# Optimization experiments

Measured on AMD Instinct MI355X. Metric: run time of the kernel, lower is better.

Reference implementation:

```python
import jax, jax.numpy as jnp
import numpy as np

B, N, L = 128, 100, 30
D_FEAT, C, CMD, T = 2112, 512, 512, 4
NEG = -1e30
INV_SQRT_C = np.float32(1.0 / np.sqrt(C))


def setup_inputs() -> dict:
    key = jax.random.key(0)
    ks = iter(jax.random.split(key, 64))

    def lin(out, inn):
        s = 1.0 / np.sqrt(inn)
        W = jax.random.uniform(next(ks), (out, inn), minval=-s, maxval=s, dtype=jnp.float32)
        b = jax.random.uniform(next(ks), (out,), minval=-s, maxval=s, dtype=jnp.float32)
        return W, b

    inp = {}
    inp['images'] = jax.random.normal(next(ks), (B, N, D_FEAT), dtype=jnp.float32)
    inp['q_encoding'] = jax.random.normal(next(ks), (B, CMD), dtype=jnp.float32)
    inp['lstm_outputs'] = jax.random.normal(next(ks), (B, L, CMD), dtype=jnp.float32)
    inp['W_initKB'], inp['b_initKB'] = lin(C, D_FEAT)
    inp['initMem'] = jax.random.normal(next(ks), (1, 1, C), dtype=jnp.float32)
    inp['W_qIn'], inp['b_qIn'] = lin(CMD, CMD)
    Ws, bs = zip(*[lin(CMD, CMD) for _ in range(T)])
    inp['W_qIn2'] = jnp.stack(Ws)
    inp['b_qIn2'] = jnp.stack(bs)
    inp['W_logit'], inp['b_logit'] = lin(1, CMD)
    inp['W_ploc'], inp['b_ploc'] = lin(C, C)
    inp['W_pctx'], inp['b_pctx'] = lin(C, C)
    inp['W_q'], inp['b_q'] = lin(C, 3 * C)
    inp['W_k'], inp['b_k'] = lin(C, 3 * C)
    inp['W_v'], inp['b_v'] = lin(C, 3 * C)
    inp['W_pk'], inp['b_pk'] = lin(C, CMD)
    inp['W_pv'], inp['b_pv'] = lin(C, CMD)
    inp['W_mem'], inp['b_mem'] = lin(C, 2 * C)
    inp['W_comb'], inp['b_comb'] = lin(C, 2 * C)
    inp['q_length'] = jax.random.randint(next(ks), (B,), 1, L + 1)
    inp['entity_num'] = jax.random.randint(next(ks), (B,), 1, N + 1)
    return inp


def _linear(x, W, b):
    return x @ W.T + b


def reference(images, q_encoding, lstm_outputs, W_initKB, b_initKB, initMem,
              W_qIn, b_qIn, W_qIn2, b_qIn2, W_logit, b_logit,
              W_ploc, b_ploc, W_pctx, b_pctx, W_q, b_q, W_k, b_k, W_v, b_v,
              W_pk, b_pk, W_pv, b_pv, W_mem, b_mem, W_comb, b_comb,
              q_length, entity_num):
    # stem (STEM_LINEAR + STEM_NORMALIZE); eval mode so dropouts + var-drop mask are identity
    imgs = images / jnp.maximum(jnp.linalg.norm(images, axis=-1, keepdims=True), 1e-12)
    x_loc = _linear(imgs, W_initKB, b_initKB)                              # [B,N,C]
    x_ctx = jnp.broadcast_to(initMem, x_loc.shape)                         # [B,N,C]
    q_mask = jnp.arange(L)[None, :] < q_length[:, None]                    # apply_mask1d [B,L]
    k_mask = jnp.arange(N)[None, None, :] < entity_num[:, None, None]      # apply_mask2d [B,1,N]
    q_cmd_base = jax.nn.elu(_linear(q_encoding, W_qIn, b_qIn))             # shared qInput layer
    for t in range(T):
        # extract textual command
        q_cmd = _linear(q_cmd_base, W_qIn2[t], b_qIn2[t])                  # [B,CMD]
        raw_att = _linear(q_cmd[:, None, :] * lstm_outputs, W_logit, b_logit)[..., 0]  # [B,L]
        att = jax.nn.softmax(jnp.where(q_mask, raw_att, NEG), axis=-1)
        cmd = jnp.einsum('bl,blc->bc', att, lstm_outputs)                  # [B,CMD]
        # propagate message
        proj_loc = _linear(x_loc, W_ploc, b_ploc)
        proj_ctx = _linear(x_ctx, W_pctx, b_pctx)
        x_joint = jnp.concatenate([x_loc, x_ctx, proj_loc * proj_ctx], axis=-1)  # [B,N,3C]
        queries = _linear(x_joint, W_q, b_q)
        keys = _linear(x_joint, W_k, b_k) * _linear(cmd, W_pk, b_pk)[:, None, :]
        vals = _linear(x_joint, W_v, b_v) * _linear(cmd, W_pv, b_pv)[:, None, :]
        scores = jnp.einsum('bqc,bkc->bqk', queries, keys) * INV_SQRT_C    # [B,N,N]
        prob = jax.nn.softmax(jnp.where(k_mask, scores, NEG), axis=-1)
        message = jnp.einsum('bqk,bkc->bqc', prob, vals)
        x_ctx = _linear(jnp.concatenate([x_ctx, message], axis=-1), W_mem, b_mem)
    return _linear(jnp.concatenate([x_loc, x_ctx], axis=-1), W_comb, b_comb)
```

## Files before the change

### kernel.cpp

```cpp
#include <hip/hip_runtime.h>
#include <math.h>

#define BB 128
#define NN 100
#define LL 30
#define CC 512
#define DFEAT 2112
#define TT 4
#define ROWS (BB * NN)
#define XJLD 1536
#define INV_SQRT_C_F 0.04419417382415922f
#define QH 50
#define VTK 128

typedef __attribute__((ext_vector_type(8))) short short8;
typedef __attribute__((ext_vector_type(4))) float f32x4;

__device__ inline unsigned short f2bf(float f) {
    unsigned u = __float_as_uint(f);
    u += 0x7fff + ((u >> 16) & 1);
    return (unsigned short)(u >> 16);
}
__device__ inline float b2f(unsigned short h) { return __uint_as_float((unsigned)h << 16); }

__device__ inline void async_ld16(const unsigned short* g, unsigned short* l) {
    __builtin_amdgcn_global_load_lds((const __attribute__((address_space(1))) void*)g,
                                     (__attribute__((address_space(3))) void*)l, 16, 0, 0);
}

__global__ __launch_bounds__(256) void rownorm_kernel(const float* __restrict__ img,
                                                      float* __restrict__ inv_norm) {
    int r = blockIdx.x;
    const float* p = img + (size_t)r * DFEAT;
    float s = 0.f;
    for (int i = threadIdx.x; i < DFEAT; i += 256) { float v = p[i]; s += v * v; }
    __shared__ float red[4];
    int lane = threadIdx.x & 63, wid = threadIdx.x >> 6;
#pragma unroll
    for (int off = 32; off > 0; off >>= 1) s += __shfl_down(s, off);
    if (lane == 0) red[wid] = s;
    __syncthreads();
    if (threadIdx.x == 0) {
        float tot = red[0] + red[1] + red[2] + red[3];
        inv_norm[r] = 1.f / fmaxf(sqrtf(tot), 1e-12f);
    }
}

__global__ __launch_bounds__(256) void cvt_kernel(const float* __restrict__ s,
                                                  unsigned short* __restrict__ d, int n4) {
    int i = blockIdx.x * blockDim.x + threadIdx.x;
    if (i < n4) {
        float4 v = ((const float4*)s)[i];
        ushort4 o;
        o.x = f2bf(v.x); o.y = f2bf(v.y); o.z = f2bf(v.z); o.w = f2bf(v.w);
        ((ushort4*)d)[i] = o;
    }
}

__global__ void zero16_kernel(uint4* __restrict__ p, int n) {
    int i = blockIdx.x * blockDim.x + threadIdx.x;
    if (i < n) p[i] = uint4{0u, 0u, 0u, 0u};
}

__global__ void bcast_kernel(const float* __restrict__ m, unsigned short* __restrict__ x) {
    int i = blockIdx.x * blockDim.x + threadIdx.x;
    if (i < ROWS * CC) {
        int r = i >> 9, c = i & (CC - 1);
        x[(size_t)r * XJLD + CC + c] = f2bf(m[c]);
    }
}

template <int MODE, bool AF32, bool OUTF32, bool DUAL, bool VT>
__global__ __launch_bounds__(256) void gemm_mfma(
    const void* __restrict__ A_, int lda,
    const unsigned short* __restrict__ W, int ldw,
    const float* __restrict__ bias,
    void* __restrict__ C_, int ldc,
    void* __restrict__ C2_,
    int K,
    const float* __restrict__ arsc,
    const float* __restrict__ rowscale) {
    __shared__ unsigned short As[128 * 64];
    __shared__ unsigned short Bs[128 * 64];
    const int t = threadIdx.x;
    const int l = t & 63;
    const int wv = t >> 6;
    const int wr = wv >> 1, wc = wv & 1;
    const int lg = l >> 4, lm = l & 15;
    const int nwg = gridDim.x;
    const int qq = nwg >> 3, rr = nwg & 7;
    const int xcd = blockIdx.x & 7, idx = blockIdx.x >> 3;
    const int wgid = (xcd < rr ? xcd * (qq + 1) : rr * (qq + 1) + (xcd - rr) * qq) + idx;
    const int m0 = (wgid >> 2) * 128, n0 = (wgid & 3) * 128;

    f32x4 acc[4][4];
#pragma unroll
    for (int mi = 0; mi < 4; ++mi)
#pragma unroll
        for (int ni = 0; ni < 4; ++ni) acc[mi][ni] = {0.f, 0.f, 0.f, 0.f};

    for (int k0 = 0; k0 < K; k0 += 64) {
        if (AF32) {
            const float* Af = (const float*)A_;
            int row = t >> 1, half = t & 1;
            const float* s = Af + (size_t)(m0 + row) * lda + k0 + half * 32;
            float sc = arsc ? arsc[m0 + row] : 1.f;
#pragma unroll
            for (int c = 0; c < 4; ++c) {
                float4 v0 = *(const float4*)(s + c * 8);
                float4 v1 = *(const float4*)(s + c * 8 + 4);
                short8 h;
                h[0] = (short)f2bf(v0.x * sc); h[1] = (short)f2bf(v0.y * sc);
                h[2] = (short)f2bf(v0.z * sc); h[3] = (short)f2bf(v0.w * sc);
                h[4] = (short)f2bf(v1.x * sc); h[5] = (short)f2bf(v1.y * sc);
                h[6] = (short)f2bf(v1.z * sc); h[7] = (short)f2bf(v1.w * sc);
                int cs = half * 4 + c;
                *(short8*)&As[row * 64 + ((cs ^ (row & 7)) * 8)] = h;
            }
        } else {
            const unsigned short* Ah = (const unsigned short*)A_;
#pragma unroll
            for (int i = 0; i < 4; ++i) {
                int lin = t + i * 256;
                int row = lin >> 3, seg = lin & 7;
                async_ld16(Ah + (size_t)(m0 + row) * lda + k0 + ((seg ^ (row & 7)) * 8),
                           &As[lin * 8]);
            }
        }
#pragma unroll
        for (int i = 0; i < 4; ++i) {
            int lin = t + i * 256;
            int row = lin >> 3, seg = lin & 7;
            async_ld16(W + (size_t)(n0 + row) * ldw + k0 + ((seg ^ (row & 7)) * 8),
                       &Bs[lin * 8]);
        }
        __syncthreads();

#pragma unroll
        for (int kk = 0; kk < 2; ++kk) {
            short8 af[4], bq[4];
#pragma unroll
            for (int mi = 0; mi < 4; ++mi) {
                int row = wr * 64 + mi * 16 + lm;
                int cs = kk * 4 + lg;
                af[mi] = *(const short8*)&As[row * 64 + ((cs ^ (row & 7)) * 8)];
            }
#pragma unroll
            for (int ni = 0; ni < 4; ++ni) {
                int row = wc * 64 + ni * 16 + lm;
                int cs = kk * 4 + lg;
                bq[ni] = *(const short8*)&Bs[row * 64 + ((cs ^ (row & 7)) * 8)];
            }
#pragma unroll
            for (int mi = 0; mi < 4; ++mi)
#pragma unroll
                for (int ni = 0; ni < 4; ++ni)
                    acc[mi][ni] = __builtin_amdgcn_mfma_f32_16x16x32_bf16(af[mi], bq[ni], acc[mi][ni], 0, 0, 0);
        }
        __syncthreads();
    }

#pragma unroll
    for (int mi = 0; mi < 4; ++mi) {
        int rbase = m0 + wr * 64 + mi * 16 + lg * 4;
#pragma unroll
        for (int ni = 0; ni < 4; ++ni) {
            int n = n0 + wc * 64 + ni * 16 + lm;
            float bv = bias[n];
#pragma unroll
            for (int j = 0; j < 4; ++j) {
                int r = rbase + j;
                float v = acc[mi][ni][j] + bv;
                size_t off = (size_t)r * ldc + n;
                if (MODE == 2) v *= b2f(((const unsigned short*)C_)[off]);
                if (MODE == 3) v *= rowscale[(size_t)(r / NN) * CC + n];
                if (OUTF32) {
                    ((float*)C_)[off] = v;
                } else {
                    unsigned short hv = f2bf(v);
                    if (VT) {
                        int b2 = r / NN, rl = r - b2 * NN;
                        ((unsigned short*)C_)[((size_t)b2 * CC + n) * VTK + rl] = hv;
                    } else {
                        ((unsigned short*)C_)[off] = hv;
                        if (DUAL) ((unsigned short*)C2_)[off] = hv;
                    }
                }
            }
        }
    }
}

template <int MODE>
__global__ __launch_bounds__(256) void gemm_small(
    const float* __restrict__ A, const float* __restrict__ W,
    const float* __restrict__ bias, float* __restrict__ C) {
    __shared__ float As[32 * 72];
    __shared__ float Bs[32 * 72];
    const int t = threadIdx.x;
    const int m0 = blockIdx.x * 64, n0 = blockIdx.y * 64;
    const int tr = t >> 4, tc = t & 15;
    float acc[4][4];
#pragma unroll
    for (int i = 0; i < 4; ++i)
#pragma unroll
        for (int j = 0; j < 4; ++j) acc[i][j] = 0.f;

    for (int k0 = 0; k0 < CC; k0 += 32) {
        int row = t >> 2, seg = t & 3;
        {
            const float* s = A + (size_t)(m0 + row) * CC + k0 + seg * 8;
            float4 v0 = *(const float4*)s, v1 = *(const float4*)(s + 4);
            As[(seg * 8 + 0) * 72 + row] = v0.x; As[(seg * 8 + 1) * 72 + row] = v0.y;
            As[(seg * 8 + 2) * 72 + row] = v0.z; As[(seg * 8 + 3) * 72 + row] = v0.w;
            As[(seg * 8 + 4) * 72 + row] = v1.x; As[(seg * 8 + 5) * 72 + row] = v1.y;
            As[(seg * 8 + 6) * 72 + row] = v1.z; As[(seg * 8 + 7) * 72 + row] = v1.w;
        }
        {
            const float* s = W + (size_t)(n0 + row) * CC + k0 + seg * 8;
            float4 v0 = *(const float4*)s, v1 = *(const float4*)(s + 4);
            Bs[(seg * 8 + 0) * 72 + row] = v0.x; Bs[(seg * 8 + 1) * 72 + row] = v0.y;
            Bs[(seg * 8 + 2) * 72 + row] = v0.z; Bs[(seg * 8 + 3) * 72 + row] = v0.w;
            Bs[(seg * 8 + 4) * 72 + row] = v1.x; Bs[(seg * 8 + 5) * 72 + row] = v1.y;
            Bs[(seg * 8 + 6) * 72 + row] = v1.z; Bs[(seg * 8 + 7) * 72 + row] = v1.w;
        }
        __syncthreads();
#pragma unroll
        for (int kk = 0; kk < 32; ++kk) {
            float4 a = *(const float4*)&As[kk * 72 + tr * 4];
            float4 b = *(const float4*)&Bs[kk * 72 + tc * 4];
            float av[4] = {a.x, a.y, a.z, a.w}, bv[4] = {b.x, b.y, b.z, b.w};
#pragma unroll
            for (int i = 0; i < 4; ++i)
#pragma unroll
                for (int j = 0; j < 4; ++j) acc[i][j] = fmaf(av[i], bv[j], acc[i][j]);
        }
        __syncthreads();
    }
#pragma unroll
    for (int i = 0; i < 4; ++i) {
#pragma unroll
        for (int j = 0; j < 4; ++j) {
            int n = n0 + tc * 4 + j;
            float v = acc[i][j] + bias[n];
            if (MODE == 4) v = v > 0.f ? v : expm1f(v);
            C[(size_t)(m0 + tr * 4 + i) * CC + n] = v;
        }
    }
}

__global__ __launch_bounds__(256) void cmd_kernel(
    const float* __restrict__ qcmd, const float* __restrict__ lstm,
    const float* __restrict__ wlogit, const float* __restrict__ blogit,
    const int* __restrict__ qlen, float* __restrict__ cmd) {
    const int b = blockIdx.x;
    const int t = threadIdx.x;
    __shared__ float qw[CC];
    __shared__ float att[LL];
    for (int c = t; c < CC; c += 256) qw[c] = qcmd[b * CC + c] * wlogit[c];
    __syncthreads();
    const int wid = t >> 6, lane = t & 63;
    for (int l = wid; l < LL; l += 4) {
        const float* lp = lstm + ((size_t)b * LL + l) * CC;
        float s = 0.f;
        for (int c = lane; c < CC; c += 64) s = fmaf(qw[c], lp[c], s);
#pragma unroll
        for (int off = 32; off > 0; off >>= 1) s += __shfl_down(s, off);
        if (lane == 0) att[l] = s + blogit[0];
    }
    __syncthreads();
    if (t == 0) {
        int Lq = qlen[b];
        float mx = -1e30f;
        for (int l = 0; l < LL; ++l) {
            if (l >= Lq) att[l] = -1e30f;
            mx = fmaxf(mx, att[l]);
        }
        float sum = 0.f;
        for (int l = 0; l < LL; ++l) { float e = expf(att[l] - mx); att[l] = e; sum += e; }
        float inv = 1.f / sum;
        for (int l = 0; l < LL; ++l) att[l] *= inv;
    }
    __syncthreads();
    for (int c = t; c < CC; c += 256) {
        float s = 0.f;
        for (int l = 0; l < LL; ++l) s = fmaf(att[l], lstm[((size_t)b * LL + l) * CC + c], s);
        cmd[b * CC + c] = s;
    }
}

__global__ __launch_bounds__(256) void attn_mfma_kernel(
    const unsigned short* __restrict__ Qm, const unsigned short* __restrict__ Km,
    const unsigned short* __restrict__ Vt, const int* __restrict__ entnum,
    unsigned short* __restrict__ msg) {
    __shared__ char ldsraw[64 * 132 * 4];
    float* S = (float*)ldsraw;
    unsigned short* Qs = (unsigned short*)ldsraw;
    unsigned short* Ks = (unsigned short*)(ldsraw + 8192);
    const int b = blockIdx.x;
    const int qbase = blockIdx.y * QH;
    const int t = threadIdx.x;
    const int wv = t >> 6, l = t & 63, lg = l >> 4, lm = l & 15;
    const unsigned short* Qp = Qm + ((size_t)b * NN + qbase) * CC;
    const unsigned short* Kp = Km + (size_t)b * NN * CC;

    f32x4 sacc[7];
#pragma unroll
    for (int i = 0; i < 7; ++i) sacc[i] = {0.f, 0.f, 0.f, 0.f};

    for (int k0 = 0; k0 < CC; k0 += 64) {
#pragma unroll
        for (int i = 0; i < 2; ++i) {
            int lin = t + i * 256;
            int row = lin >> 3, seg = lin & 7;
            async_ld16(Qp + (size_t)row * CC + k0 + ((seg ^ (row & 7)) * 8), &Qs[lin * 8]);
        }
#pragma unroll
        for (int i = 0; i < 4; ++i) {
            int lin = t + i * 256;
            if (lin < 896) {
                int row = lin >> 3, seg = lin & 7;
                async_ld16(Kp + (size_t)row * CC + k0 + ((seg ^ (row & 7)) * 8), &Ks[lin * 8]);
            }
        }
        __syncthreads();
#pragma unroll
        for (int kk = 0; kk < 2; ++kk) {
            int arow = wv * 16 + lm;
            int cs = kk * 4 + lg;
            short8 a = *(const short8*)&Qs[arow * 64 + ((cs ^ (arow & 7)) * 8)];
#pragma unroll
            for (int nf = 0; nf < 7; ++nf) {
                int brow = nf * 16 + lm;
                short8 bb = *(const short8*)&Ks[brow * 64 + ((cs ^ (brow & 7)) * 8)];
                sacc[nf] = __builtin_amdgcn_mfma_f32_16x16x32_bf16(a, bb, sacc[nf], 0, 0, 0);
            }
        }
        __syncthreads();
    }
#pragma unroll
    for (int nf = 0; nf < 7; ++nf)
#pragma unroll
        for (int j = 0; j < 4; ++j)
            S[(wv * 16 + lg * 4 + j) * 132 + nf * 16 + lm] = sacc[nf][j] * INV_SQRT_C_F;
    __syncthreads();

    const int en = entnum[b];
    for (int q = wv; q < QH; q += 4) {
        float v0 = (l < en) ? S[q * 132 + l] : -1e30f;
        int k1 = l + 64;
        float v1 = (k1 < en) ? S[q * 132 + k1] : -1e30f;
        float mx = fmaxf(v0, v1);
#pragma unroll
        for (int o = 32; o > 0; o >>= 1) mx = fmaxf(mx, __shfl_xor(mx, o));
        float e0 = (l < en) ? expf(v0 - mx) : 0.f;
        float e1 = (k1 < en) ? expf(v1 - mx) : 0.f;
        float ss = e0 + e1;
#pragma unroll
        for (int o = 32; o > 0; o >>= 1) ss += __shfl_xor(ss, o);
        float inv = 1.f / ss;
        S[q * 132 + l] = e0 * inv;
        S[q * 132 + k1] = e1 * inv;
    }
    __syncthreads();

    f32x4 acc[4][8];
#pragma unroll
    for (int mf = 0; mf < 4; ++mf)
#pragma unroll
        for (int nf = 0; nf < 8; ++nf) acc[mf][nf] = {0.f, 0.f, 0.f, 0.f};

    const unsigned short* Vb = Vt + (size_t)b * CC * VTK;
    for (int ks = 0; ks < 4; ++ks) {
        int k0 = ks * 32;
        short8 pa[4];
#pragma unroll
        for (int mf = 0; mf < 4; ++mf) {
            const float* sp = &S[(mf * 16 + lm) * 132 + k0 + lg * 8];
            short8 h;
#pragma unroll
            for (int jj = 0; jj < 8; ++jj) h[jj] = (short)f2bf(sp[jj]);
            pa[mf] = h;
        }
#pragma unroll
        for (int nf = 0; nf < 8; ++nf) {
            short8 bb = *(const short8*)(Vb + ((size_t)(wv * 128 + nf * 16 + lm)) * VTK + k0 + lg * 8);
#pragma unroll
            for (int mf = 0; mf < 4; ++mf)
                acc[mf][nf] = __builtin_amdgcn_mfma_f32_16x16x32_bf16(pa[mf], bb, acc[mf][nf], 0, 0, 0);
        }
    }
#pragma unroll
    for (int mf = 0; mf < 4; ++mf) {
#pragma unroll
        for (int j = 0; j < 4; ++j) {
            int q = mf * 16 + lg * 4 + j;
            if (q < QH) {
                size_t rb = ((size_t)b * NN + qbase + q) * XJLD;
#pragma unroll
                for (int nf = 0; nf < 8; ++nf)
                    msg[rb + wv * 128 + nf * 16 + lm] = f2bf(acc[mf][nf][j]);
            }
        }
    }
}

extern "C" void kernel_launch(void* const* d_in, const int* in_sizes, int n_in,
                              void* d_out, int out_size, void* d_ws, size_t ws_size,
                              hipStream_t stream) {
    const float* images   = (const float*)d_in[0];
    const float* q_enc    = (const float*)d_in[1];
    const float* lstm     = (const float*)d_in[2];
    const float* W_initKB = (const float*)d_in[3];
    const float* b_initKB = (const float*)d_in[4];
    const float* initMem  = (const float*)d_in[5];
    const float* W_qIn    = (const float*)d_in[6];
    const float* b_qIn    = (const float*)d_in[7];
    const float* W_qIn2   = (const float*)d_in[8];
    const float* b_qIn2   = (const float*)d_in[9];
    const float* W_logit  = (const float*)d_in[10];
    const float* b_logit  = (const float*)d_in[11];
    const float* W_ploc   = (const float*)d_in[12];
    const float* b_ploc   = (const float*)d_in[13];
    const float* W_pctx   = (const float*)d_in[14];
    const float* b_pctx   = (const float*)d_in[15];
    const float* W_q      = (const float*)d_in[16];
    const float* b_q      = (const float*)d_in[17];
    const float* W_k      = (const float*)d_in[18];
    const float* b_k      = (const float*)d_in[19];
    const float* W_v      = (const float*)d_in[20];
    const float* b_v      = (const float*)d_in[21];
    const float* W_pk     = (const float*)d_in[22];
    const float* b_pk     = (const float*)d_in[23];
    const float* W_pv     = (const float*)d_in[24];
    const float* b_pv     = (const float*)d_in[25];
    const float* W_mem    = (const float*)d_in[26];
    const float* b_mem    = (const float*)d_in[27];
    const float* W_comb   = (const float*)d_in[28];
    const float* b_comb   = (const float*)d_in[29];
    const int* q_length   = (const int*)d_in[30];
    const int* entity_num = (const int*)d_in[31];
    (void)in_sizes; (void)n_in; (void)out_size; (void)ws_size;

    char* p = (char*)d_ws;
    auto alloc = [&](size_t bytes) { char* q = p; p += (bytes + 255) & ~(size_t)255; return q; };
    unsigned short* XJ0 = (unsigned short*)alloc((size_t)ROWS * XJLD * 2);
    unsigned short* XJ1 = (unsigned short*)alloc((size_t)ROWS * XJLD * 2);
    unsigned short* Qb  = (unsigned short*)alloc((size_t)ROWS * CC * 2);
    unsigned short* Kb  = (unsigned short*)alloc((size_t)ROWS * CC * 2);
    unsigned short* Vt  = (unsigned short*)alloc((size_t)BB * CC * VTK * 2);
    unsigned short* Wbf = (unsigned short*)alloc((size_t)5013504 * 2);
    float* qcb  = (float*)alloc((size_t)BB * CC * 4);
    float* qcmd = (float*)alloc((size_t)BB * CC * 4);
    float* cmd  = (float*)alloc((size_t)BB * CC * 4);
    float* pk   = (float*)alloc((size_t)BB * CC * 4);
    float* pv   = (float*)alloc((size_t)BB * CC * 4);
    float* invn = (float*)alloc((size_t)ROWS * 4);

    unsigned short* Wi_init = Wbf + 0;
    unsigned short* Wi_ploc = Wbf + 1081344;
    unsigned short* Wi_pctx = Wbf + 1343488;
    unsigned short* Wi_q    = Wbf + 1605632;
    unsigned short* Wi_k    = Wbf + 2392064;
    unsigned short* Wi_v    = Wbf + 3178496;
    unsigned short* Wi_mem  = Wbf + 3964928;
    unsigned short* Wi_comb = Wbf + 4489216;

    auto cvt = [&](const float* src, unsigned short* dst, size_t n) {
        int n4 = (int)(n / 4);
        cvt_kernel<<<dim3((n4 + 255) / 256), dim3(256), 0, stream>>>(src, dst, n4);
    };

    rownorm_kernel<<<dim3(ROWS), dim3(256), 0, stream>>>(images, invn);
    zero16_kernel<<<dim3(((int)((size_t)BB * CC * VTK * 2 / 16) + 255) / 256), dim3(256), 0, stream>>>(
        (uint4*)Vt, (int)((size_t)BB * CC * VTK * 2 / 16));
    cvt(W_initKB, Wi_init, (size_t)CC * DFEAT);
    cvt(W_ploc,  Wi_ploc, (size_t)CC * CC);
    cvt(W_pctx,  Wi_pctx, (size_t)CC * CC);
    cvt(W_q,     Wi_q,    (size_t)CC * 3 * CC);
    cvt(W_k,     Wi_k,    (size_t)CC * 3 * CC);
    cvt(W_v,     Wi_v,    (size_t)CC * 3 * CC);
    cvt(W_mem,   Wi_mem,  (size_t)CC * 2 * CC);
    cvt(W_comb,  Wi_comb, (size_t)CC * 2 * CC);

    dim3 gBig((ROWS / 128) * 4), blk(256);
    gemm_mfma<0, true, false, true, false><<<gBig, blk, 0, stream>>>(
        images, DFEAT, Wi_init, DFEAT, b_initKB, XJ0, XJLD, XJ1, DFEAT, invn, nullptr);
    bcast_kernel<<<dim3((ROWS * CC + 255) / 256), dim3(256), 0, stream>>>(initMem, XJ0);
    gemm_small<4><<<dim3(BB / 64, 8), blk, 0, stream>>>(q_enc, W_qIn, b_qIn, qcb);

    for (int t = 0; t < TT; ++t) {
        unsigned short* R  = (t & 1) ? XJ1 : XJ0;
        unsigned short* Wr = (t & 1) ? XJ0 : XJ1;
        gemm_small<0><<<dim3(BB / 64, 8), blk, 0, stream>>>(
            qcb, W_qIn2 + (size_t)t * CC * CC, b_qIn2 + (size_t)t * CC, qcmd);
        cmd_kernel<<<dim3(BB), blk, 0, stream>>>(qcmd, lstm, W_logit, b_logit, q_length, cmd);
        gemm_small<0><<<dim3(BB / 64, 8), blk, 0, stream>>>(cmd, W_pk, b_pk, pk);
        gemm_small<0><<<dim3(BB / 64, 8), blk, 0, stream>>>(cmd, W_pv, b_pv, pv);
        gemm_mfma<0, false, false, false, false><<<gBig, blk, 0, stream>>>(
            R, XJLD, Wi_ploc, CC, b_ploc, R + 2 * CC, XJLD, nullptr, CC, nullptr, nullptr);
        gemm_mfma<2, false, false, false, false><<<gBig, blk, 0, stream>>>(
            R + CC, XJLD, Wi_pctx, CC, b_pctx, R + 2 * CC, XJLD, nullptr, CC, nullptr, nullptr);
        gemm_mfma<0, false, false, false, false><<<gBig, blk, 0, stream>>>(
            R, XJLD, Wi_q, 3 * CC, b_q, Qb, CC, nullptr, 3 * CC, nullptr, nullptr);
        gemm_mfma<3, false, false, false, false><<<gBig, blk, 0, stream>>>(
            R, XJLD, Wi_k, 3 * CC, b_k, Kb, CC, nullptr, 3 * CC, nullptr, pk);
        gemm_mfma<3, false, false, false, true><<<gBig, blk, 0, stream>>>(
            R, XJLD, Wi_v, 3 * CC, b_v, Vt, CC, nullptr, 3 * CC, nullptr, pv);
        attn_mfma_kernel<<<dim3(BB, 2), blk, 0, stream>>>(Qb, Kb, Vt, entity_num, R + 2 * CC);
        gemm_mfma<0, false, false, false, false><<<gBig, blk, 0, stream>>>(
            R + CC, XJLD, Wi_mem, 2 * CC, b_mem, Wr + CC, XJLD, nullptr, 2 * CC, nullptr, nullptr);
    }
    gemm_mfma<0, false, true, false, false><<<gBig, blk, 0, stream>>>(
        XJ0, XJLD, Wi_comb, 2 * CC, b_comb, (float*)d_out, CC, nullptr, 2 * CC, nullptr, nullptr);
}
```

Baseline: 1.575 ms.

## Fuse ploc/pctx product GEMM, merge Q/K/V GEMMs, add double-buffered LDS

The ploc and pctx projections now run in one kernel that keeps two accumulators and writes their product directly, so the separate read-modify-write pass is gone. The Q, K and V projections become a single launch with a 12-way tile split, which removes launch gaps and gives a larger grid. The bf16 GEMMs now double-buffer LDS staging so the next K tile loads while the current one computes. The cost is twice the LDS per block and, in the product kernel, twice the accumulator registers, which may lower occupancy.

Result: no change. 1.569 ms (-0.4%).

```diff
diff --git a/kernel.cpp b/kernel.cpp
--- a/kernel.cpp
+++ b/kernel.cpp
@@ -28,6 +28,12 @@
                                      (__attribute__((address_space(3))) void*)l, 16, 0, 0);
 }
 
+__device__ inline int xcd_swz(int bid, int nwg) {
+    int qq = nwg >> 3, rr = nwg & 7;
+    int xcd = bid & 7, idx = bid >> 3;
+    return (xcd < rr ? xcd * (qq + 1) : rr * (qq + 1) + (xcd - rr) * qq) + idx;
+}
+
 __global__ __launch_bounds__(256) void rownorm_kernel(const float* __restrict__ img,
                                                       float* __restrict__ inv_norm) {
     int r = blockIdx.x;
@@ -70,16 +76,275 @@
     }
 }
 
-template <int MODE, bool AF32, bool OUTF32, bool DUAL, bool VT>
-__global__ __launch_bounds__(256) void gemm_mfma(
-    const void* __restrict__ A_, int lda,
+template <int EPI>
+__global__ __launch_bounds__(256) void gemm_dbuf(
+    const unsigned short* __restrict__ A, int lda,
     const unsigned short* __restrict__ W, int ldw,
     const float* __restrict__ bias,
-    void* __restrict__ C_, int ldc,
-    void* __restrict__ C2_,
-    int K,
-    const float* __restrict__ arsc,
-    const float* __restrict__ rowscale) {
+    void* __restrict__ C_, int ldc, int K) {
+    __shared__ unsigned short As[2][128 * 64];
+    __shared__ unsigned short Bs[2][128 * 64];
+    const int t = threadIdx.x;
+    const int l = t & 63;
+    const int wv = t >> 6;
+    const int wr = wv >> 1, wc = wv & 1;
+    const int lg = l >> 4, lm = l & 15;
+    const int wgid = xcd_swz(blockIdx.x, gridDim.x);
+    const int m0 = (wgid >> 2) * 128, n0 = (wgid & 3) * 128;
+
+    f32x4 acc[4][4];
+#pragma unroll
+    for (int mi = 0; mi < 4; ++mi)
+#pragma unroll
+        for (int ni = 0; ni < 4; ++ni) acc[mi][ni] = {0.f, 0.f, 0.f, 0.f};
+
+    auto stage = [&](int buf, int k0) {
+#pragma unroll
+        for (int i = 0; i < 4; ++i) {
+            int lin = t + i * 256;
+            int row = lin >> 3, seg = lin & 7;
+            async_ld16(A + (size_t)(m0 + row) * lda + k0 + ((seg ^ (row & 7)) * 8),
+                       &As[buf][lin * 8]);
+            async_ld16(W + (size_t)(n0 + row) * ldw + k0 + ((seg ^ (row & 7)) * 8),
+                       &Bs[buf][lin * 8]);
+        }
+    };
+
+    const int nk = K >> 6;
+    stage(0, 0);
+    __syncthreads();
+    for (int kt = 0; kt < nk; ++kt) {
+        int cur = kt & 1;
+        if (kt + 1 < nk) stage(cur ^ 1, (kt + 1) * 64);
+#pragma unroll
+        for (int kk = 0; kk < 2; ++kk) {
+            short8 af[4], bq[4];
+#pragma unroll
+            for (int mi = 0; mi < 4; ++mi) {
+                int row = wr * 64 + mi * 16 + lm;
+                int cs = kk * 4 + lg;
+                af[mi] = *(const short8*)&As[cur][row * 64 + ((cs ^ (row & 7)) * 8)];
+            }
+#pragma unroll
+            for (int ni = 0; ni < 4; ++ni) {
+                int row = wc * 64 + ni * 16 + lm;
+                int cs = kk * 4 + lg;
+                bq[ni] = *(const short8*)&Bs[cur][row * 64 + ((cs ^ (row & 7)) * 8)];
+            }
+#pragma unroll
+            for (int mi = 0; mi < 4; ++mi)
+#pragma unroll
+                for (int ni = 0; ni < 4; ++ni)
+                    acc[mi][ni] = __builtin_amdgcn_mfma_f32_16x16x32_bf16(af[mi], bq[ni], acc[mi][ni], 0, 0, 0);
+        }
+        __syncthreads();
+    }
+
+#pragma unroll
+    for (int mi = 0; mi < 4; ++mi) {
+        int rbase = m0 + wr * 64 + mi * 16 + lg * 4;
+#pragma unroll
+        for (int ni = 0; ni < 4; ++ni) {
+            int n = n0 + wc * 64 + ni * 16 + lm;
+            float bv = bias[n];
+#pragma unroll
+            for (int j = 0; j < 4; ++j) {
+                int r = rbase + j;
+                float v = acc[mi][ni][j] + bv;
+                if (EPI == 1) ((float*)C_)[(size_t)r * ldc + n] = v;
+                else ((unsigned short*)C_)[(size_t)r * ldc + n] = f2bf(v);
+            }
+        }
+    }
+}
+
+__global__ __launch_bounds__(256) void gemm_qkv(
+    const unsigned short* __restrict__ A,
+    const unsigned short* __restrict__ Wq, const unsigned short* __restrict__ Wk,
+    const unsigned short* __restrict__ Wv,
+    const float* __restrict__ bq_, const float* __restrict__ bk_,
+    const float* __restrict__ bv_,
+    unsigned short* __restrict__ Qb, unsigned short* __restrict__ Kb,
+    unsigned short* __restrict__ Vt,
+    const float* __restrict__ pk, const float* __restrict__ pv) {
+    __shared__ unsigned short As[2][128 * 64];
+    __shared__ unsigned short Bs[2][128 * 64];
+    const int t = threadIdx.x;
+    const int l = t & 63;
+    const int wv_ = t >> 6;
+    const int wr = wv_ >> 1, wc = wv_ & 1;
+    const int lg = l >> 4, lm = l & 15;
+    const int wgid = xcd_swz(blockIdx.x, gridDim.x);
+    const int mtile = wgid / 12, sub = wgid - mtile * 12;
+    const int op = sub >> 2;
+    const int m0 = mtile * 128, n0 = (sub & 3) * 128;
+    const unsigned short* W = (op == 0) ? Wq : (op == 1) ? Wk : Wv;
+    const float* bias = (op == 0) ? bq_ : (op == 1) ? bk_ : bv_;
+
+    f32x4 acc[4][4];
+#pragma unroll
+    for (int mi = 0; mi < 4; ++mi)
+#pragma unroll
+        for (int ni = 0; ni < 4; ++ni) acc[mi][ni] = {0.f, 0.f, 0.f, 0.f};
+
+    auto stage = [&](int buf, int k0) {
+#pragma unroll
+        for (int i = 0; i < 4; ++i) {
+            int lin = t + i * 256;
+            int row = lin >> 3, seg = lin & 7;
+            async_ld16(A + (size_t)(m0 + row) * XJLD + k0 + ((seg ^ (row & 7)) * 8),
+                       &As[buf][lin * 8]);
+            async_ld16(W + (size_t)(n0 + row) * XJLD + k0 + ((seg ^ (row & 7)) * 8),
+                       &Bs[buf][lin * 8]);
+        }
+    };
+
+    const int nk = XJLD >> 6;
+    stage(0, 0);
+    __syncthreads();
+    for (int kt = 0; kt < nk; ++kt) {
+        int cur = kt & 1;
+        if (kt + 1 < nk) stage(cur ^ 1, (kt + 1) * 64);
+#pragma unroll
+        for (int kk = 0; kk < 2; ++kk) {
+            short8 af[4], bqf[4];
+#pragma unroll
+            for (int mi = 0; mi < 4; ++mi) {
+                int row = wr * 64 + mi * 16 + lm;
+                int cs = kk * 4 + lg;
+                af[mi] = *(const short8*)&As[cur][row * 64 + ((cs ^ (row & 7)) * 8)];
+            }
+#pragma unroll
+            for (int ni = 0; ni < 4; ++ni) {
+                int row = wc * 64 + ni * 16 + lm;
+                int cs = kk * 4 + lg;
+                bqf[ni] = *(const short8*)&Bs[cur][row * 64 + ((cs ^ (row & 7)) * 8)];
+            }
+#pragma unroll
+            for (int mi = 0; mi < 4; ++mi)
+#pragma unroll
+                for (int ni = 0; ni < 4; ++ni)
+                    acc[mi][ni] = __builtin_amdgcn_mfma_f32_16x16x32_bf16(af[mi], bqf[ni], acc[mi][ni], 0, 0, 0);
+        }
+        __syncthreads();
+    }
+
+#pragma unroll
+    for (int mi = 0; mi < 4; ++mi) {
+        int rbase = m0 + wr * 64 + mi * 16 + lg * 4;
+#pragma unroll
+        for (int ni = 0; ni < 4; ++ni) {
+            int n = n0 + wc * 64 + ni * 16 + lm;
+            float bv2 = bias[n];
+#pragma unroll
+            for (int j = 0; j < 4; ++j) {
+                int r = rbase + j;
+                float v = acc[mi][ni][j] + bv2;
+                if (op == 0) {
+                    Qb[(size_t)r * CC + n] = f2bf(v);
+                } else if (op == 1) {
+                    v *= pk[(size_t)(r / NN) * CC + n];
+                    Kb[(size_t)r * CC + n] = f2bf(v);
+                } else {
+                    v *= pv[(size_t)(r / NN) * CC + n];
+                    int b2 = r / NN, rl = r - b2 * NN;
+                    Vt[((size_t)b2 * CC + n) * VTK + rl] = f2bf(v);
+                }
+            }
+        }
+    }
+}
+
+__global__ __launch_bounds__(256) void gemm_prod(
+    const unsigned short* __restrict__ Aloc, const unsigned short* __restrict__ Actx,
+    const unsigned short* __restrict__ W0, const unsigned short* __restrict__ W1,
+    const float* __restrict__ b0, const float* __restrict__ b1,
+    unsigned short* __restrict__ C) {
+    __shared__ unsigned short A0s[2][128 * 32];
+    __shared__ unsigned short A1s[2][128 * 32];
+    __shared__ unsigned short B0s[2][128 * 32];
+    __shared__ unsigned short B1s[2][128 * 32];
+    const int t = threadIdx.x;
+    const int l = t & 63;
+    const int wv = t >> 6;
+    const int wr = wv >> 1, wc = wv & 1;
+    const int lg = l >> 4, lm = l & 15;
+    const int wgid = xcd_swz(blockIdx.x, gridDim.x);
+    const int m0 = (wgid >> 2) * 128, n0 = (wgid & 3) * 128;
+
+    f32x4 a0[4][4], a1[4][4];
+#pragma unroll
+    for (int mi = 0; mi < 4; ++mi)
+#pragma unroll
+        for (int ni = 0; ni < 4; ++ni) { a0[mi][ni] = {0.f,0.f,0.f,0.f}; a1[mi][ni] = {0.f,0.f,0.f,0.f}; }
+
+    auto stage = [&](int buf, int k0) {
+#pragma unroll
+        for (int i = 0; i < 2; ++i) {
+            int lin = t + i * 256;
+            int row = lin >> 2, seg = lin & 3;
+            int goff = k0 + ((seg ^ ((row >> 1) & 3)) * 8);
+            async_ld16(Aloc + (size_t)(m0 + row) * XJLD + goff, &A0s[buf][lin * 8]);
+            async_ld16(Actx + (size_t)(m0 + row) * XJLD + goff, &A1s[buf][lin * 8]);
+            async_ld16(W0 + (size_t)(n0 + row) * CC + goff, &B0s[buf][lin * 8]);
+            async_ld16(W1 + (size_t)(n0 + row) * CC + goff, &B1s[buf][lin * 8]);
+        }
+    };
+
+    const int nk = CC >> 5;
+    stage(0, 0);
+    __syncthreads();
+    for (int kt = 0; kt < nk; ++kt) {
+        int cur = kt & 1;
+        if (kt + 1 < nk) stage(cur ^ 1, (kt + 1) * 32);
+        short8 af0[4], af1[4], bf0[4], bf1[4];
+#pragma unroll
+        for (int mi = 0; mi < 4; ++mi) {
+            int row = wr * 64 + mi * 16 + lm;
+            int off = row * 32 + ((lg ^ ((row >> 1) & 3)) * 8);
+            af0[mi] = *(const short8*)&A0s[cur][off];
+            af1[mi] = *(const short8*)&A1s[cur][off];
+        }
+#pragma unroll
+        for (int ni = 0; ni < 4; ++ni) {
+            int row = wc * 64 + ni * 16 + lm;
+            int off = row * 32 + ((lg ^ ((row >> 1) & 3)) * 8);
+            bf0[ni] = *(const short8*)&B0s[cur][off];
+            bf1[ni] = *(const short8*)&B1s[cur][off];
+        }
+#pragma unroll
+        for (int mi = 0; mi < 4; ++mi)
+#pragma unroll
+            for (int ni = 0; ni < 4; ++ni) {
+                a0[mi][ni] = __builtin_amdgcn_mfma_f32_16x16x32_bf16(af0[mi], bf0[ni], a0[mi][ni], 0, 0, 0);
+                a1[mi][ni] = __builtin_amdgcn_mfma_f32_16x16x32_bf16(af1[mi], bf1[ni], a1[mi][ni], 0, 0, 0);
+            }
+        __syncthreads();
+    }
+
+#pragma unroll
+    for (int mi = 0; mi < 4; ++mi) {
+        int rbase = m0 + wr * 64 + mi * 16 + lg * 4;
+#pragma unroll
+        for (int ni = 0; ni < 4; ++ni) {
+            int n = n0 + wc * 64 + ni * 16 + lm;
+            float bv0 = b0[n], bv1 = b1[n];
+#pragma unroll
+            for (int j = 0; j < 4; ++j) {
+                int r = rbase + j;
+                float v = (a0[mi][ni][j] + bv0) * (a1[mi][ni][j] + bv1);
+                C[(size_t)r * XJLD + n] = f2bf(v);
+            }
+        }
+    }
+}
+
+__global__ __launch_bounds__(256) void gemm_stem(
+    const float* __restrict__ Af, int lda,
+    const unsigned short* __restrict__ W, int ldw,
+    const float* __restrict__ bias,
+    unsigned short* __restrict__ C0, unsigned short* __restrict__ C1,
+    int K, const float* __restrict__ arsc) {
     __shared__ unsigned short As[128 * 64];
     __shared__ unsigned short Bs[128 * 64];
     const int t = threadIdx.x;
@@ -87,10 +352,7 @@
     const int wv = t >> 6;
     const int wr = wv >> 1, wc = wv & 1;
     const int lg = l >> 4, lm = l & 15;
-    const int nwg = gridDim.x;
-    const int qq = nwg >> 3, rr = nwg & 7;
-    const int xcd = blockIdx.x & 7, idx = blockIdx.x >> 3;
-    const int wgid = (xcd < rr ? xcd * (qq + 1) : rr * (qq + 1) + (xcd - rr) * qq) + idx;
+    const int wgid = xcd_swz(blockIdx.x, gridDim.x);
     const int m0 = (wgid >> 2) * 128, n0 = (wgid & 3) * 128;
 
     f32x4 acc[4][4];
@@ -100,11 +362,10 @@
         for (int ni = 0; ni < 4; ++ni) acc[mi][ni] = {0.f, 0.f, 0.f, 0.f};
 
     for (int k0 = 0; k0 < K; k0 += 64) {
-        if (AF32) {
-            const float* Af = (const float*)A_;
+        {
             int row = t >> 1, half = t & 1;
             const float* s = Af + (size_t)(m0 + row) * lda + k0 + half * 32;
-            float sc = arsc ? arsc[m0 + row] : 1.f;
+            float sc = arsc[m0 + row];
 #pragma unroll
             for (int c = 0; c < 4; ++c) {
                 float4 v0 = *(const float4*)(s + c * 8);
@@ -117,15 +378,6 @@
                 int cs = half * 4 + c;
                 *(short8*)&As[row * 64 + ((cs ^ (row & 7)) * 8)] = h;
             }
-        } else {
-            const unsigned short* Ah = (const unsigned short*)A_;
-#pragma unroll
-            for (int i = 0; i < 4; ++i) {
-                int lin = t + i * 256;
-                int row = lin >> 3, seg = lin & 7;
-                async_ld16(Ah + (size_t)(m0 + row) * lda + k0 + ((seg ^ (row & 7)) * 8),
-                           &As[lin * 8]);
-            }
         }
 #pragma unroll
         for (int i = 0; i < 4; ++i) {
@@ -135,7 +387,6 @@
                        &Bs[lin * 8]);
         }
         __syncthreads();
-
 #pragma unroll
         for (int kk = 0; kk < 2; ++kk) {
             short8 af[4], bq[4];
@@ -159,7 +410,6 @@
         }
         __syncthreads();
     }
-
 #pragma unroll
     for (int mi = 0; mi < 4; ++mi) {
         int rbase = m0 + wr * 64 + mi * 16 + lg * 4;
@@ -170,22 +420,9 @@
 #pragma unroll
             for (int j = 0; j < 4; ++j) {
                 int r = rbase + j;
-                float v = acc[mi][ni][j] + bv;
-                size_t off = (size_t)r * ldc + n;
-                if (MODE == 2) v *= b2f(((const unsigned short*)C_)[off]);
-                if (MODE == 3) v *= rowscale[(size_t)(r / NN) * CC + n];
-                if (OUTF32) {
-                    ((float*)C_)[off] = v;
-                } else {
-                    unsigned short hv = f2bf(v);
-                    if (VT) {
-                        int b2 = r / NN, rl = r - b2 * NN;
-                        ((unsigned short*)C_)[((size_t)b2 * CC + n) * VTK + rl] = hv;
-                    } else {
-                        ((unsigned short*)C_)[off] = hv;
-                        if (DUAL) ((unsigned short*)C2_)[off] = hv;
-                    }
-                }
+                unsigned short hv = f2bf(acc[mi][ni][j] + bv);
+                C0[(size_t)r * XJLD + n] = hv;
+                C1[(size_t)r * XJLD + n] = hv;
             }
         }
     }
@@ -483,9 +720,10 @@
     cvt(W_mem,   Wi_mem,  (size_t)CC * 2 * CC);
     cvt(W_comb,  Wi_comb, (size_t)CC * 2 * CC);
 
-    dim3 gBig((ROWS / 128) * 4), blk(256);
-    gemm_mfma<0, true, false, true, false><<<gBig, blk, 0, stream>>>(
-        images, DFEAT, Wi_init, DFEAT, b_initKB, XJ0, XJLD, XJ1, DFEAT, invn, nullptr);
+    dim3 blk(256);
+    dim3 g400((ROWS / 128) * 4);
+    gemm_stem<<<g400, blk, 0, stream>>>(images, DFEAT, Wi_init, DFEAT, b_initKB,
+                                        XJ0, XJ1, DFEAT, invn);
     bcast_kernel<<<dim3((ROWS * CC + 255) / 256), dim3(256), 0, stream>>>(initMem, XJ0);
     gemm_small<4><<<dim3(BB / 64, 8), blk, 0, stream>>>(q_enc, W_qIn, b_qIn, qcb);
 
@@ -497,20 +735,14 @@
         cmd_kernel<<<dim3(BB), blk, 0, stream>>>(qcmd, lstm, W_logit, b_logit, q_length, cmd);
         gemm_small<0><<<dim3(BB / 64, 8), blk, 0, stream>>>(cmd, W_pk, b_pk, pk);
         gemm_small<0><<<dim3(BB / 64, 8), blk, 0, stream>>>(cmd, W_pv, b_pv, pv);
-        gemm_mfma<0, false, false, false, false><<<gBig, blk, 0, stream>>>(
-            R, XJLD, Wi_ploc, CC, b_ploc, R + 2 * CC, XJLD, nullptr, CC, nullptr, nullptr);
-        gemm_mfma<2, false, false, false, false><<<gBig, blk, 0, stream>>>(
-            R + CC, XJLD, Wi_pctx, CC, b_pctx, R + 2 * CC, XJLD, nullptr, CC, nullptr, nullptr);
-        gemm_mfma<0, false, false, false, false><<<gBig, blk, 0, stream>>>(
-            R, XJLD, Wi_q, 3 * CC, b_q, Qb, CC, nullptr, 3 * CC, nullptr, nullptr);
-        gemm_mfma<3, false, false, false, false><<<gBig, blk, 0, stream>>>(
-            R, XJLD, Wi_k, 3 * CC, b_k, Kb, CC, nullptr, 3 * CC, nullptr, pk);
-        gemm_mfma<3, false, false, false, true><<<gBig, blk, 0, stream>>>(
-            R, XJLD, Wi_v, 3 * CC, b_v, Vt, CC, nullptr, 3 * CC, nullptr, pv);
+        gemm_prod<<<g400, blk, 0, stream>>>(R, R + CC, Wi_ploc, Wi_pctx,
+                                            b_ploc, b_pctx, R + 2 * CC);
+        gemm_qkv<<<dim3((ROWS / 128) * 12), blk, 0, stream>>>(
+            R, Wi_q, Wi_k, Wi_v, b_q, b_k, b_v, Qb, Kb, Vt, pk, pv);
         attn_mfma_kernel<<<dim3(BB, 2), blk, 0, stream>>>(Qb, Kb, Vt, entity_num, R + 2 * CC);
-        gemm_mfma<0, false, false, false, false><<<gBig, blk, 0, stream>>>(
-            R + CC, XJLD, Wi_mem, 2 * CC, b_mem, Wr + CC, XJLD, nullptr, 2 * CC, nullptr, nullptr);
-    }
-    gemm_mfma<0, false, true, false, false><<<gBig, blk, 0, stream>>>(
-        XJ0, XJLD, Wi_comb, 2 * CC, b_comb, (float*)d_out, CC, nullptr, 2 * CC, nullptr, nullptr);
-}
+        gemm_dbuf<0><<<g400, blk, 0, stream>>>(R + CC, XJLD, Wi_mem, 2 * CC, b_mem,
+                                               Wr + CC, XJLD, 2 * CC);
+    }
+    gemm_dbuf<1><<<g400, blk, 0, stream>>>(XJ0, XJLD, Wi_comb, 2 * CC, b_comb,
+                                           (float*)d_out, CC, 2 * CC);
+}
```
